# Optimization experiments

Hardware: AMD Instinct MI355X
Metric: run time of the kernel (lower is better)

The kernel has to match this reference:

```python
import jax, jax.numpy as jnp
import numpy as np

N = 8388608      # number of points
S = 32768        # number of superpoints (segments)


def setup_inputs() -> dict:
    key = jax.random.key(0)
    k1, k2, k3 = jax.random.split(key, 3)
    pos = jax.random.normal(k1, (N, 3), dtype=jnp.float32)
    idx = jnp.sort(jax.random.randint(k2, (N,), 0, S, dtype=jnp.int64))
    w = jax.random.uniform(k3, (N,), dtype=jnp.float32)  # non-negative weights
    return {"pos": pos, "idx": idx, "w": w, "num_super": S}


def reference(pos, idx, w, num_super):
    # Per-segment min / max of coordinates: [S, 3]
    mn = jax.ops.segment_min(pos, idx, num_segments=num_super, indices_are_sorted=True)
    mx = jax.ops.segment_max(pos, idx, num_segments=num_super, indices_are_sorted=True)
    # Per-segment diameter = largest coordinate extent: [S]
    diameter_segment = (mx - mn).max(axis=1)
    # Weighted per-segment center: sum(w*pos) / sum(w), guarding zero-weight segments
    w_sum = jax.ops.segment_sum(w, idx, num_segments=num_super, indices_are_sorted=True)
    w_sum_safe = jnp.where(w_sum == 0, 1.0, w_sum)
    center_segment = (
        jax.ops.segment_sum(pos * w[:, None], idx, num_segments=num_super,
                            indices_are_sorted=True)
        / w_sum_safe[:, None]
    )
    # Gather per-node center/diameter and normalize into unit sphere
    pos_out = (pos - center_segment[idx]) / (diameter_segment[idx][:, None] + 0.01)
    return pos_out, diameter_segment.reshape(-1, 1)
```

## Files before the change

### kernel.cpp

```cpp
#include <hip/hip_runtime.h>

#define WAVE 64
#define SPB 4

__global__ void detect_idx64(const unsigned int* __restrict__ w32, long long N,
                             int* __restrict__ flag) {
    long long base = (N / 2) | 1LL;
    long long stride = ((N / 2) / 64) & ~1LL;
    if (stride < 2) stride = 2;
    long long p = base + (long long)threadIdx.x * stride;
    unsigned int v = (p < N) ? w32[p] : 0u;
    unsigned long long nz = __ballot(v != 0u);
    if (threadIdx.x == 0) *flag = (nz == 0ULL) ? 1 : 0;
}

__device__ __forceinline__ int load_idx(const void* __restrict__ p,
                                        long long i, int is64) {
    return is64 ? (int)((const long long*)p)[i] : ((const int*)p)[i];
}

__global__ void find_bounds(const void* __restrict__ idxp,
                            const int* __restrict__ flag,
                            int* __restrict__ start,
                            long long N, int S) {
    long long b = ((long long)blockIdx.x * blockDim.x + threadIdx.x) << 2;
    if (b >= N) return;
    const int is64 = *flag;
    int prev = (b == 0) ? -1 : load_idx(idxp, b - 1, is64);
    #pragma unroll
    for (int k = 0; k < 4; ++k) {
        long long i = b + k;
        if (i >= N) break;
        int cur = load_idx(idxp, i, is64);
        for (int s = prev + 1; s <= cur; ++s) start[s] = (int)i;
        prev = cur;
    }
    if (b + 4 >= N)
        for (int s = prev + 1; s <= S; ++s) start[s] = (int)N;
}

__global__ __launch_bounds__(SPB * WAVE)
void seg_norm(const float* __restrict__ pos,
              const float* __restrict__ w,
              const int* __restrict__ start,
              float* __restrict__ out,
              float* __restrict__ diam_out,
              int S) {
    const int s = blockIdx.x * SPB + (threadIdx.x >> 6);
    if (s >= S) return;
    const int lane = threadIdx.x & 63;

    const int lo = start[s], hi = start[s + 1];
    const int g0 = lo >> 2, g1 = (hi + 3) >> 2;

    const float4* __restrict__ pos4 = (const float4*)pos;
    const float4* __restrict__ w4   = (const float4*)w;

    const int ga = g0 + lane;
    const int gb = ga + WAVE;
    const bool va = ga < g1, vb = gb < g1;

    float4 a0 = {0,0,0,0}, a1 = {0,0,0,0}, a2 = {0,0,0,0}, aw = {0,0,0,0};
    float4 b0 = {0,0,0,0}, b1 = {0,0,0,0}, b2 = {0,0,0,0}, bw = {0,0,0,0};
    if (va) {
        a0 = pos4[3LL * ga]; a1 = pos4[3LL * ga + 1]; a2 = pos4[3LL * ga + 2];
        aw = w4[ga];
    }
    if (vb) {
        b0 = pos4[3LL * gb]; b1 = pos4[3LL * gb + 1]; b2 = pos4[3LL * gb + 2];
        bw = w4[gb];
    }

    float mnx = INFINITY,  mny = INFINITY,  mnz = INFINITY;
    float mxx = -INFINITY, mxy = -INFINITY, mxz = -INFINITY;
    float sw = 0.f, swx = 0.f, swy = 0.f, swz = 0.f;

    #define PROC(PI, X, Y, Z, WV)                                        \
    {                                                                    \
        bool in = ((PI) >= lo) & ((PI) < hi);                            \
        float xv = (X), yv = (Y), zv = (Z);                              \
        float wv = in ? (WV) : 0.f;                                      \
        mnx = fminf(mnx, in ? xv :  INFINITY);                           \
        mxx = fmaxf(mxx, in ? xv : -INFINITY);                           \
        mny = fminf(mny, in ? yv :  INFINITY);                           \
        mxy = fmaxf(mxy, in ? yv : -INFINITY);                           \
        mnz = fminf(mnz, in ? zv :  INFINITY);                           \
        mxz = fmaxf(mxz, in ? zv : -INFINITY);                           \
        sw += wv;                                                        \
        swx = fmaf(wv, xv, swx);                                         \
        swy = fmaf(wv, yv, swy);                                         \
        swz = fmaf(wv, zv, swz);                                         \
    }
    #define PROC_GROUP(G, R0, R1, R2, RW)                                \
    {                                                                    \
        const int p = (G) << 2;                                          \
        PROC(p + 0, R0.x, R0.y, R0.z, RW.x)                              \
        PROC(p + 1, R0.w, R1.x, R1.y, RW.y)                              \
        PROC(p + 2, R1.z, R1.w, R2.x, RW.z)                              \
        PROC(p + 3, R2.y, R2.z, R2.w, RW.w)                              \
    }

    PROC_GROUP(ga, a0, a1, a2, aw)
    PROC_GROUP(gb, b0, b1, b2, bw)

    for (int g = g0 + 2 * WAVE + lane; g < g1; g += WAVE) {
        float4 c0 = pos4[3LL * g], c1 = pos4[3LL * g + 1], c2 = pos4[3LL * g + 2];
        float4 cw = w4[g];
        PROC_GROUP(g, c0, c1, c2, cw)
    }

    #pragma unroll
    for (int off = 1; off < WAVE; off <<= 1) {
        mnx = fminf(mnx, __shfl_xor(mnx, off));
        mny = fminf(mny, __shfl_xor(mny, off));
        mnz = fminf(mnz, __shfl_xor(mnz, off));
        mxx = fmaxf(mxx, __shfl_xor(mxx, off));
        mxy = fmaxf(mxy, __shfl_xor(mxy, off));
        mxz = fmaxf(mxz, __shfl_xor(mxz, off));
        sw  += __shfl_xor(sw,  off);
        swx += __shfl_xor(swx, off);
        swy += __shfl_xor(swy, off);
        swz += __shfl_xor(swz, off);
    }

    const float diam = fmaxf(mxx - mnx, fmaxf(mxy - mny, mxz - mnz));
    const float wsafe = (sw == 0.f) ? 1.f : sw;
    const float cx = swx / wsafe, cy = swy / wsafe, cz = swz / wsafe;
    const float inv = 1.f / (diam + 0.01f);
    if (lane == 0) diam_out[s] = diam;

    float4* __restrict__ out4 = (float4*)out;

    #define STORE_GROUP(G, R0, R1, R2)                                       \
    {                                                                        \
        const int p = (G) << 2;                                              \
        float4 ra, rb, rc;                                                   \
        ra.x = (R0.x - cx) * inv; ra.y = (R0.y - cy) * inv;                  \
        ra.z = (R0.z - cz) * inv; ra.w = (R0.w - cx) * inv;                  \
        rb.x = (R1.x - cy) * inv; rb.y = (R1.y - cz) * inv;                  \
        rb.z = (R1.z - cx) * inv; rb.w = (R1.w - cy) * inv;                  \
        rc.x = (R2.x - cz) * inv; rc.y = (R2.y - cx) * inv;                  \
        rc.z = (R2.z - cy) * inv; rc.w = (R2.w - cz) * inv;                  \
        if (p >= lo && p + 4 <= hi) {                                        \
            out4[3LL * (G)] = ra; out4[3LL * (G) + 1] = rb;                  \
            out4[3LL * (G) + 2] = rc;                                        \
        } else {                                                             \
            const long long f = 12LL * (G);                                  \
            if (p + 0 >= lo && p + 0 < hi) {                                 \
                out[f + 0] = ra.x; out[f + 1]  = ra.y; out[f + 2]  = ra.z;   \
            }                                                                \
            if (p + 1 >= lo && p + 1 < hi) {                                 \
                out[f + 3] = ra.w; out[f + 4]  = rb.x; out[f + 5]  = rb.y;   \
            }                                                                \
            if (p + 2 >= lo && p + 2 < hi) {                                 \
                out[f + 6] = rb.z; out[f + 7]  = rb.w; out[f + 8]  = rc.x;   \
            }                                                                \
            if (p + 3 >= lo && p + 3 < hi) {                                 \
                out[f + 9] = rc.y; out[f + 10] = rc.z; out[f + 11] = rc.w;   \
            }                                                                \
        }                                                                    \
    }

    STORE_GROUP(ga, a0, a1, a2)
    STORE_GROUP(gb, b0, b1, b2)

    for (int g = g0 + 2 * WAVE + lane; g < g1; g += WAVE) {
        float4 c0 = pos4[3LL * g], c1 = pos4[3LL * g + 1], c2 = pos4[3LL * g + 2];
        STORE_GROUP(g, c0, c1, c2)
    }

    #undef STORE_GROUP
    #undef PROC_GROUP
    #undef PROC
}

extern "C" void kernel_launch(void* const* d_in, const int* in_sizes, int n_in,
                              void* d_out, int out_size, void* d_ws, size_t ws_size,
                              hipStream_t stream) {
    const float* pos  = (const float*)d_in[0];
    const void*  idxp = d_in[1];
    const float* w    = (const float*)d_in[2];

    const long long N = (long long)in_sizes[0] / 3;
    const int S = out_size - in_sizes[0];

    float* out = (float*)d_out;
    float* diam_out = out + (long long)in_sizes[0];

    int* flag  = (int*)d_ws;
    int* start = (int*)((char*)d_ws + 256);

    detect_idx64<<<1, 64, 0, stream>>>((const unsigned int*)idxp, N, flag);

    const long long nt4 = (N + 3) >> 2;
    find_bounds<<<(int)((nt4 + 255) / 256), 256, 0, stream>>>(idxp, flag, start, N, S);

    seg_norm<<<(S + SPB - 1) / SPB, SPB * WAVE, 0, stream>>>(
        pos, w, start, out, diam_out, S);
}
```

Baseline: 61.01 us.

## Vectorize bounds loads, add persistent segment loop and nontemporal output stores

find_bounds now loads four indices with one vector load and gets each lane's predecessor index through a wave shuffle, so it no longer re-reads neighbouring indices. seg_norm becomes a grid-stride persistent kernel capped at 2048 blocks, with each wave looping over segments. Its second-tile processing is skipped when no lane in the wave needs it, and full output groups are written with nontemporal stores. The aim is to cut redundant global loads and launch overhead and to keep streaming output out of the cache. The cost is fewer blocks in flight to hide memory latency.

```diff
diff --git a/kernel.cpp b/kernel.cpp
--- a/kernel.cpp
+++ b/kernel.cpp
@@ -2,6 +2,7 @@
 
 #define WAVE 64
 #define SPB 4
+typedef float v4f __attribute__((ext_vector_type(4)));
 
 __global__ void detect_idx64(const unsigned int* __restrict__ w32, long long N,
                              int* __restrict__ flag) {
@@ -23,20 +24,43 @@
                             const int* __restrict__ flag,
                             int* __restrict__ start,
                             long long N, int S) {
-    long long b = ((long long)blockIdx.x * blockDim.x + threadIdx.x) << 2;
-    if (b >= N) return;
+    const long long b = ((long long)blockIdx.x * blockDim.x + threadIdx.x) << 2;
+    const bool active = b < N;
     const int is64 = *flag;
-    int prev = (b == 0) ? -1 : load_idx(idxp, b - 1, is64);
-    #pragma unroll
-    for (int k = 0; k < 4; ++k) {
-        long long i = b + k;
-        if (i >= N) break;
-        int cur = load_idx(idxp, i, is64);
-        for (int s = prev + 1; s <= cur; ++s) start[s] = (int)i;
-        prev = cur;
+
+    int v0 = 0, v1 = 0, v2 = 0, v3 = 0;
+    int nval = 0;
+    if (active) {
+        if (b + 4 <= N) {
+            nval = 4;
+            if (is64) {
+                const longlong2* p = (const longlong2*)((const long long*)idxp + b);
+                longlong2 q0 = p[0], q1 = p[1];
+                v0 = (int)q0.x; v1 = (int)q0.y; v2 = (int)q1.x; v3 = (int)q1.y;
+            } else {
+                int4 q = *(const int4*)((const int*)idxp + b);
+                v0 = q.x; v1 = q.y; v2 = q.z; v3 = q.w;
+            }
+        } else {
+            nval = (int)(N - b);
+            v0 = load_idx(idxp, b, is64);
+            if (nval > 1) v1 = load_idx(idxp, b + 1, is64);
+            if (nval > 2) v2 = load_idx(idxp, b + 2, is64);
+        }
     }
-    if (b + 4 >= N)
-        for (int s = prev + 1; s <= S; ++s) start[s] = (int)N;
+    int last = (nval == 4) ? v3 : (nval == 3) ? v2 : (nval == 2) ? v1 : v0;
+    int prev = __shfl_up(last, 1);
+    if ((threadIdx.x & 63) == 0)
+        prev = (b == 0) ? -1 : (active ? load_idx(idxp, b - 1, is64) : 0);
+    if (!active) return;
+
+    int c = prev;
+    if (nval >= 1) { if (v0 > c) { for (int t = c + 1; t <= v0; ++t) start[t] = (int)(b);     } c = v0; }
+    if (nval >= 2) { if (v1 > c) { for (int t = c + 1; t <= v1; ++t) start[t] = (int)(b + 1); } c = v1; }
+    if (nval >= 3) { if (v2 > c) { for (int t = c + 1; t <= v2; ++t) start[t] = (int)(b + 2); } c = v2; }
+    if (nval >= 4) { if (v3 > c) { for (int t = c + 1; t <= v3; ++t) start[t] = (int)(b + 3); } c = v3; }
+    if (b + nval >= N)
+        for (int t = c + 1; t <= S; ++t) start[t] = (int)N;
 }
 
 __global__ __launch_bounds__(SPB * WAVE)
@@ -46,132 +70,136 @@
               float* __restrict__ out,
               float* __restrict__ diam_out,
               int S) {
-    const int s = blockIdx.x * SPB + (threadIdx.x >> 6);
-    if (s >= S) return;
+    const int wid  = threadIdx.x >> 6;
     const int lane = threadIdx.x & 63;
-
-    const int lo = start[s], hi = start[s + 1];
-    const int g0 = lo >> 2, g1 = (hi + 3) >> 2;
+    const int step = gridDim.x * SPB;
 
     const float4* __restrict__ pos4 = (const float4*)pos;
     const float4* __restrict__ w4   = (const float4*)w;
-
-    const int ga = g0 + lane;
-    const int gb = ga + WAVE;
-    const bool va = ga < g1, vb = gb < g1;
-
-    float4 a0 = {0,0,0,0}, a1 = {0,0,0,0}, a2 = {0,0,0,0}, aw = {0,0,0,0};
-    float4 b0 = {0,0,0,0}, b1 = {0,0,0,0}, b2 = {0,0,0,0}, bw = {0,0,0,0};
-    if (va) {
-        a0 = pos4[3LL * ga]; a1 = pos4[3LL * ga + 1]; a2 = pos4[3LL * ga + 2];
-        aw = w4[ga];
+    float4* __restrict__ out4 = (float4*)out;
+
+    for (int s = blockIdx.x * SPB + wid; s < S; s += step) {
+        const int su = __builtin_amdgcn_readfirstlane(s);
+        const int lo = start[su], hi = start[su + 1];
+        const int g0 = lo >> 2, g1 = (hi + 3) >> 2;
+
+        const int ga = g0 + lane;
+        const int gb = ga + WAVE;
+        const bool va = ga < g1, vb = gb < g1;
+        const bool anyb = __any(vb);
+
+        float4 a0 = {0,0,0,0}, a1 = {0,0,0,0}, a2 = {0,0,0,0}, aw = {0,0,0,0};
+        float4 b0 = {0,0,0,0}, b1 = {0,0,0,0}, b2 = {0,0,0,0}, bw = {0,0,0,0};
+        if (va) {
+            a0 = pos4[3LL * ga]; a1 = pos4[3LL * ga + 1]; a2 = pos4[3LL * ga + 2];
+            aw = w4[ga];
+        }
+        if (anyb && vb) {
+            b0 = pos4[3LL * gb]; b1 = pos4[3LL * gb + 1]; b2 = pos4[3LL * gb + 2];
+            bw = w4[gb];
+        }
+
+        float mnx = INFINITY,  mny = INFINITY,  mnz = INFINITY;
+        float mxx = -INFINITY, mxy = -INFINITY, mxz = -INFINITY;
+        float sw = 0.f, swx = 0.f, swy = 0.f, swz = 0.f;
+
+        #define PROC(PI, X, Y, Z, WV)                                        \
+        {                                                                    \
+            bool in = ((PI) >= lo) & ((PI) < hi);                            \
+            float xv = (X), yv = (Y), zv = (Z);                              \
+            float wv = in ? (WV) : 0.f;                                      \
+            mnx = fminf(mnx, in ? xv :  INFINITY);                           \
+            mxx = fmaxf(mxx, in ? xv : -INFINITY);                           \
+            mny = fminf(mny, in ? yv :  INFINITY);                           \
+            mxy = fmaxf(mxy, in ? yv : -INFINITY);                           \
+            mnz = fminf(mnz, in ? zv :  INFINITY);                           \
+            mxz = fmaxf(mxz, in ? zv : -INFINITY);                           \
+            sw += wv;                                                        \
+            swx = fmaf(wv, xv, swx);                                         \
+            swy = fmaf(wv, yv, swy);                                         \
+            swz = fmaf(wv, zv, swz);                                         \
+        }
+        #define PROC_GROUP(G, R0, R1, R2, RW)                                \
+        {                                                                    \
+            const int p = (G) << 2;                                          \
+            PROC(p + 0, R0.x, R0.y, R0.z, RW.x)                              \
+            PROC(p + 1, R0.w, R1.x, R1.y, RW.y)                              \
+            PROC(p + 2, R1.z, R1.w, R2.x, RW.z)                              \
+            PROC(p + 3, R2.y, R2.z, R2.w, RW.w)                              \
+        }
+
+        PROC_GROUP(ga, a0, a1, a2, aw)
+        if (anyb) PROC_GROUP(gb, b0, b1, b2, bw)
+
+        for (int g = g0 + 2 * WAVE + lane; g < g1; g += WAVE) {
+            float4 c0 = pos4[3LL * g], c1 = pos4[3LL * g + 1], c2 = pos4[3LL * g + 2];
+            float4 cw = w4[g];
+            PROC_GROUP(g, c0, c1, c2, cw)
+        }
+
+        #pragma unroll
+        for (int off = 1; off < WAVE; off <<= 1) {
+            mnx = fminf(mnx, __shfl_xor(mnx, off));
+            mny = fminf(mny, __shfl_xor(mny, off));
+            mnz = fminf(mnz, __shfl_xor(mnz, off));
+            mxx = fmaxf(mxx, __shfl_xor(mxx, off));
+            mxy = fmaxf(mxy, __shfl_xor(mxy, off));
+            mxz = fmaxf(mxz, __shfl_xor(mxz, off));
+            sw  += __shfl_xor(sw,  off);
+            swx += __shfl_xor(swx, off);
+            swy += __shfl_xor(swy, off);
+            swz += __shfl_xor(swz, off);
+        }
+
+        const float diam = fmaxf(mxx - mnx, fmaxf(mxy - mny, mxz - mnz));
+        const float wsafe = (sw == 0.f) ? 1.f : sw;
+        const float cx = swx / wsafe, cy = swy / wsafe, cz = swz / wsafe;
+        const float inv = 1.f / (diam + 0.01f);
+        if (lane == 0) diam_out[s] = diam;
+
+        #define STORE_GROUP(G, R0, R1, R2)                                       \
+        {                                                                        \
+            const int p = (G) << 2;                                              \
+            float4 ra, rb, rc;                                                   \
+            ra.x = (R0.x - cx) * inv; ra.y = (R0.y - cy) * inv;                  \
+            ra.z = (R0.z - cz) * inv; ra.w = (R0.w - cx) * inv;                  \
+            rb.x = (R1.x - cy) * inv; rb.y = (R1.y - cz) * inv;                  \
+            rb.z = (R1.z - cx) * inv; rb.w = (R1.w - cy) * inv;                  \
+            rc.x = (R2.x - cz) * inv; rc.y = (R2.y - cx) * inv;                  \
+            rc.z = (R2.z - cy) * inv; rc.w = (R2.w - cz) * inv;                  \
+            if (p >= lo && p + 4 <= hi) {                                        \
+                __builtin_nontemporal_store(*(const v4f*)&ra, (v4f*)&out4[3LL * (G)]);     \
+                __builtin_nontemporal_store(*(const v4f*)&rb, (v4f*)&out4[3LL * (G) + 1]); \
+                __builtin_nontemporal_store(*(const v4f*)&rc, (v4f*)&out4[3LL * (G) + 2]); \
+            } else {                                                             \
+                const long long f = 12LL * (G);                                  \
+                if (p + 0 >= lo && p + 0 < hi) {                                 \
+                    out[f + 0] = ra.x; out[f + 1]  = ra.y; out[f + 2]  = ra.z;   \
+                }                                                                \
+                if (p + 1 >= lo && p + 1 < hi) {                                 \
+                    out[f + 3] = ra.w; out[f + 4]  = rb.x; out[f + 5]  = rb.y;   \
+                }                                                                \
+                if (p + 2 >= lo && p + 2 < hi) {                                 \
+                    out[f + 6] = rb.z; out[f + 7]  = rb.w; out[f + 8]  = rc.x;   \
+                }                                                                \
+                if (p + 3 >= lo && p + 3 < hi) {                                 \
+                    out[f + 9] = rc.y; out[f + 10] = rc.z; out[f + 11] = rc.w;   \
+                }                                                                \
+            }                                                                    \
+        }
+
+        STORE_GROUP(ga, a0, a1, a2)
+        if (anyb) STORE_GROUP(gb, b0, b1, b2)
+
+        for (int g = g0 + 2 * WAVE + lane; g < g1; g += WAVE) {
+            float4 c0 = pos4[3LL * g], c1 = pos4[3LL * g + 1], c2 = pos4[3LL * g + 2];
+            STORE_GROUP(g, c0, c1, c2)
+        }
+
+        #undef STORE_GROUP
+        #undef PROC_GROUP
+        #undef PROC
     }
-    if (vb) {
-        b0 = pos4[3LL * gb]; b1 = pos4[3LL * gb + 1]; b2 = pos4[3LL * gb + 2];
-        bw = w4[gb];
-    }
-
-    float mnx = INFINITY,  mny = INFINITY,  mnz = INFINITY;
-    float mxx = -INFINITY, mxy = -INFINITY, mxz = -INFINITY;
-    float sw = 0.f, swx = 0.f, swy = 0.f, swz = 0.f;
-
-    #define PROC(PI, X, Y, Z, WV)                                        \
-    {                                                                    \
-        bool in = ((PI) >= lo) & ((PI) < hi);                            \
-        float xv = (X), yv = (Y), zv = (Z);                              \
-        float wv = in ? (WV) : 0.f;                                      \
-        mnx = fminf(mnx, in ? xv :  INFINITY);                           \
-        mxx = fmaxf(mxx, in ? xv : -INFINITY);                           \
-        mny = fminf(mny, in ? yv :  INFINITY);                           \
-        mxy = fmaxf(mxy, in ? yv : -INFINITY);                           \
-        mnz = fminf(mnz, in ? zv :  INFINITY);                           \
-        mxz = fmaxf(mxz, in ? zv : -INFINITY);                           \
-        sw += wv;                                                        \
-        swx = fmaf(wv, xv, swx);                                         \
-        swy = fmaf(wv, yv, swy);                                         \
-        swz = fmaf(wv, zv, swz);                                         \
-    }
-    #define PROC_GROUP(G, R0, R1, R2, RW)                                \
-    {                                                                    \
-        const int p = (G) << 2;                                          \
-        PROC(p + 0, R0.x, R0.y, R0.z, RW.x)                              \
-        PROC(p + 1, R0.w, R1.x, R1.y, RW.y)                              \
-        PROC(p + 2, R1.z, R1.w, R2.x, RW.z)                              \
-        PROC(p + 3, R2.y, R2.z, R2.w, RW.w)                              \
-    }
-
-    PROC_GROUP(ga, a0, a1, a2, aw)
-    PROC_GROUP(gb, b0, b1, b2, bw)
-
-    for (int g = g0 + 2 * WAVE + lane; g < g1; g += WAVE) {
-        float4 c0 = pos4[3LL * g], c1 = pos4[3LL * g + 1], c2 = pos4[3LL * g + 2];
-        float4 cw = w4[g];
-        PROC_GROUP(g, c0, c1, c2, cw)
-    }
-
-    #pragma unroll
-    for (int off = 1; off < WAVE; off <<= 1) {
-        mnx = fminf(mnx, __shfl_xor(mnx, off));
-        mny = fminf(mny, __shfl_xor(mny, off));
-        mnz = fminf(mnz, __shfl_xor(mnz, off));
-        mxx = fmaxf(mxx, __shfl_xor(mxx, off));
-        mxy = fmaxf(mxy, __shfl_xor(mxy, off));
-        mxz = fmaxf(mxz, __shfl_xor(mxz, off));
-        sw  += __shfl_xor(sw,  off);
-        swx += __shfl_xor(swx, off);
-        swy += __shfl_xor(swy, off);
-        swz += __shfl_xor(swz, off);
-    }
-
-    const float diam = fmaxf(mxx - mnx, fmaxf(mxy - mny, mxz - mnz));
-    const float wsafe = (sw == 0.f) ? 1.f : sw;
-    const float cx = swx / wsafe, cy = swy / wsafe, cz = swz / wsafe;
-    const float inv = 1.f / (diam + 0.01f);
-    if (lane == 0) diam_out[s] = diam;
-
-    float4* __restrict__ out4 = (float4*)out;
-
-    #define STORE_GROUP(G, R0, R1, R2)                                       \
-    {                                                                        \
-        const int p = (G) << 2;                                              \
-        float4 ra, rb, rc;                                                   \
-        ra.x = (R0.x - cx) * inv; ra.y = (R0.y - cy) * inv;                  \
-        ra.z = (R0.z - cz) * inv; ra.w = (R0.w - cx) * inv;                  \
-        rb.x = (R1.x - cy) * inv; rb.y = (R1.y - cz) * inv;                  \
-        rb.z = (R1.z - cx) * inv; rb.w = (R1.w - cy) * inv;                  \
-        rc.x = (R2.x - cz) * inv; rc.y = (R2.y - cx) * inv;                  \
-        rc.z = (R2.z - cy) * inv; rc.w = (R2.w - cz) * inv;                  \
-        if (p >= lo && p + 4 <= hi) {                                        \
-            out4[3LL * (G)] = ra; out4[3LL * (G) + 1] = rb;                  \
-            out4[3LL * (G) + 2] = rc;                                        \
-        } else {                                                             \
-            const long long f = 12LL * (G);                                  \
-            if (p + 0 >= lo && p + 0 < hi) {                                 \
-                out[f + 0] = ra.x; out[f + 1]  = ra.y; out[f + 2]  = ra.z;   \
-            }                                                                \
-            if (p + 1 >= lo && p + 1 < hi) {                                 \
-                out[f + 3] = ra.w; out[f + 4]  = rb.x; out[f + 5]  = rb.y;   \
-            }                                                                \
-            if (p + 2 >= lo && p + 2 < hi) {                                 \
-                out[f + 6] = rb.z; out[f + 7]  = rb.w; out[f + 8]  = rc.x;   \
-            }                                                                \
-            if (p + 3 >= lo && p + 3 < hi) {                                 \
-                out[f + 9] = rc.y; out[f + 10] = rc.z; out[f + 11] = rc.w;   \
-            }                                                                \
-        }                                                                    \
-    }
-
-    STORE_GROUP(ga, a0, a1, a2)
-    STORE_GROUP(gb, b0, b1, b2)
-
-    for (int g = g0 + 2 * WAVE + lane; g < g1; g += WAVE) {
-        float4 c0 = pos4[3LL * g], c1 = pos4[3LL * g + 1], c2 = pos4[3LL * g + 2];
-        STORE_GROUP(g, c0, c1, c2)
-    }
-
-    #undef STORE_GROUP
-    #undef PROC_GROUP
-    #undef PROC
 }
 
 extern "C" void kernel_launch(void* const* d_in, const int* in_sizes, int n_in,
@@ -195,6 +223,7 @@
     const long long nt4 = (N + 3) >> 2;
     find_bounds<<<(int)((nt4 + 255) / 256), 256, 0, stream>>>(idxp, flag, start, N, S);
 
-    seg_norm<<<(S + SPB - 1) / SPB, SPB * WAVE, 0, stream>>>(
-        pos, w, start, out, diam_out, S);
-}
+    int sgrid = (S + SPB - 1) / SPB;
+    int grid = sgrid < 2048 ? sgrid : 2048;
+    seg_norm<<<grid, SPB * WAVE, 0, stream>>>(pos, w, start, out, diam_out, S);
+}
```

Result: slower. 65.54 us (+7.4%).
